# Performance work log

Measured on AMD Instinct MI355X. Metric: run time of the kernel, lower is better.

Reference implementation:

```python
import jax, jax.numpy as jnp
import numpy as np

DIM = 2048
HEADS = 32
WINDOW = 8   # local_attn
B = 4
N = 197


def _local_mask(w, n):
    # Faithful to local_attention(): for row i, columns j in [max(i-w,0), min(i+w, n))
    # get weight (w - |i-j|/2)/w; everything else is 0 (later masked to -inf).
    i = jnp.arange(n)[:, None]
    j = jnp.arange(n)[None, :]
    d = jnp.abs(i - j).astype(jnp.float32)
    in_win = (j >= i - w) & (j < i + w)  # range(start, end) excludes i+w
    return jnp.where(in_win, (w - d / 2.0) / w, 0.0)  # (N, N)


def setup_inputs() -> dict:
    key = jax.random.key(0)
    k1, k2, k3, k4 = jax.random.split(key, 4)
    x = jax.random.normal(k1, (B, N, DIM), dtype=jnp.float32)
    qkv_w = jax.random.normal(k2, (3 * DIM, DIM), dtype=jnp.float32) * 0.02  # no qkv bias
    proj_w = jax.random.normal(k3, (DIM, DIM), dtype=jnp.float32) * 0.02
    proj_b = jax.random.normal(k4, (DIM,), dtype=jnp.float32) * 0.02
    return {"x": x, "qkv_w": qkv_w, "proj_w": proj_w, "proj_b": proj_b}


def reference(x, qkv_w, proj_w, proj_b):
    Bb, Nn, C = x.shape
    H = HEADS
    hd = C // H
    scale = hd ** (-0.5)
    # qkv projection: (B, N, 3C) -> (3, B, H, N, hd)
    qkv = (x @ qkv_w.T).reshape(Bb, Nn, 3, H, hd).transpose(2, 0, 3, 1, 4)
    q, k, v = qkv[0], qkv[1], qkv[2]
    attn = jnp.einsum('bhnd,bhmd->bhnm', q, k) * scale  # (B, H, N, N)
    m = _local_mask(WINDOW, Nn)  # (N, N), broadcasts over B, H
    # attn * mask, then masked_fill(mask == 0, -inf), then softmax
    attn = jnp.where(m != 0.0, attn * m, -jnp.inf)
    attn = jax.nn.softmax(attn, axis=-1)
    out = jnp.einsum('bhnm,bhmd->bhnd', attn, v)  # (B, H, N, hd)
    out = out.transpose(0, 2, 1, 3).reshape(Bb, Nn, C)
    return out @ proj_w.T + proj_b
```

## Files before the change

kernel.cpp:

```cpp
#include <hip/hip_runtime.h>
#include <math.h>

#define B_SZ   4
#define N_SEQ  197
#define DIMC   2048
#define HEADS  32
#define HD     64
#define WIN    8
#define M_ROWS (B_SZ * N_SEQ)
#define M_PAD  896

using f32x4 = __attribute__((ext_vector_type(4))) float;
using s16x8 = __attribute__((ext_vector_type(8))) short;

__device__ inline ushort f2bf(float f) {
  uint x = __float_as_uint(f);
  uint r = (x + 0x7fffu + ((x >> 16) & 1u)) >> 16;
  return (ushort)r;
}
__device__ inline float bf2f(ushort u) {
  return __uint_as_float(((uint)u) << 16);
}

__device__ inline void gload16(const ushort* g, ushort* l) {
  __builtin_amdgcn_global_load_lds(
      (const __attribute__((address_space(1))) unsigned int*)g,
      (__attribute__((address_space(3))) unsigned int*)l, 16, 0, 0);
}

#define NX (M_ROWS * DIMC / 8)
#define NQ (3 * DIMC * DIMC / 8)
#define NP (DIMC * DIMC / 8)

__global__ __launch_bounds__(256)
void cvt_all(const float* __restrict__ x,  const float* __restrict__ qw,
             const float* __restrict__ pw, ushort* __restrict__ xb,
             ushort* __restrict__ qwb, ushort* __restrict__ pwb) {
  int i = blockIdx.x * 256 + threadIdx.x;
  const float* src; ushort* dst; int idx;
  if (i < NX)                { src = x;  dst = xb;  idx = i; }
  else if (i < NX + NQ)      { src = qw; dst = qwb; idx = i - NX; }
  else if (i < NX + NQ + NP) { src = pw; dst = pwb; idx = i - NX - NQ; }
  else return;
  f32x4 a = ((const f32x4*)src)[2 * idx];
  f32x4 b = ((const f32x4*)src)[2 * idx + 1];
  ushort4 u0, u1;
  u0.x = f2bf(a.x); u0.y = f2bf(a.y); u0.z = f2bf(a.z); u0.w = f2bf(a.w);
  u1.x = f2bf(b.x); u1.y = f2bf(b.y); u1.z = f2bf(b.z); u1.w = f2bf(b.w);
  ((ushort4*)dst)[2 * idx]     = u0;
  ((ushort4*)dst)[2 * idx + 1] = u1;
}

__global__ __launch_bounds__(256, 3)
void gemm_bt_bf16(const ushort* __restrict__ A, const ushort* __restrict__ Bw,
                  ushort* __restrict__ Cout,
                  int Mdim, int Ndim, int Kfull, int Ksplit) {
  __shared__ ushort As[3][128 * 32];
  __shared__ ushort Bs[3][128 * 32];
  const int tid  = threadIdx.x;
  const int lane = tid & 63;
  const int wave = tid >> 6;

  const int nwg  = gridDim.x * gridDim.y;
  const int phys = blockIdx.y * gridDim.x + blockIdx.x;
  const int cpx  = nwg >> 3;
  const int lg   = (phys & 7) * cpx + (phys >> 3);
  const int m0 = (lg % gridDim.x) * 128;
  const int n0 = (lg / gridDim.x) * 128;
  const int koff = blockIdx.z * Ksplit;
  ushort* C = Cout + (size_t)blockIdx.z * Mdim * Ndim;

  const int wr = (wave >> 1) * 64;
  const int wc = (wave & 1) * 64;
  const int fr = lane & 15;
  const int kg = lane >> 4;
  const int srow = lane >> 2;
  const int scol = ((lane & 3) ^ ((srow >> 1) & 3)) * 8;
  const int rdA  = (kg ^ ((fr >> 1) & 3)) * 8;

  f32x4 acc[4][4];
#pragma unroll
  for (int i = 0; i < 4; ++i)
#pragma unroll
    for (int j = 0; j < 4; ++j)
      acc[i][j] = (f32x4){0.f, 0.f, 0.f, 0.f};

  const ushort* Asrc0 = A  + (size_t)(m0 + wave * 32 + srow)      * Kfull + koff + scol;
  const ushort* Asrc1 = A  + (size_t)(m0 + wave * 32 + 16 + srow) * Kfull + koff + scol;
  const ushort* Bsrc0 = Bw + (size_t)(n0 + wave * 32 + srow)      * Kfull + koff + scol;
  const ushort* Bsrc1 = Bw + (size_t)(n0 + wave * 32 + 16 + srow) * Kfull + koff + scol;

  const int nt = Ksplit >> 5;

  auto STAGE = [&](int kk, int b) {
    const int k = kk << 5;
    gload16(Asrc0 + k, &As[b][wave * 1024]);
    gload16(Asrc1 + k, &As[b][wave * 1024 + 512]);
    gload16(Bsrc0 + k, &Bs[b][wave * 1024]);
    gload16(Bsrc1 + k, &Bs[b][wave * 1024 + 512]);
  };

  STAGE(0, 0);
  STAGE(1, 1);

  int cur = 0, s2 = 2;
  for (int t = 0; t < nt; ++t) {
    if (t < nt - 1) asm volatile("s_waitcnt vmcnt(4)" ::: "memory");
    else            asm volatile("s_waitcnt vmcnt(0)" ::: "memory");
    __builtin_amdgcn_s_barrier();
    __builtin_amdgcn_sched_barrier(0);

    if (t + 2 < nt) STAGE(t + 2, s2);

    s16x8 af[4], bfr[4];
#pragma unroll
    for (int i = 0; i < 4; ++i)
      af[i] = *(const s16x8*)(&As[cur][(wr + i * 16 + fr) * 32 + rdA]);
#pragma unroll
    for (int j = 0; j < 4; ++j)
      bfr[j] = *(const s16x8*)(&Bs[cur][(wc + j * 16 + fr) * 32 + rdA]);
    __builtin_amdgcn_s_setprio(1);
#pragma unroll
    for (int i = 0; i < 4; ++i)
#pragma unroll
      for (int j = 0; j < 4; ++j)
        acc[i][j] = __builtin_amdgcn_mfma_f32_16x16x32_bf16(af[i], bfr[j], acc[i][j], 0, 0, 0);
    __builtin_amdgcn_s_setprio(0);

    cur += 1; if (cur >= 3) cur -= 3;
    s2  += 1; if (s2  >= 3) s2  -= 3;
  }

  const int crow_base = m0 + wr + kg * 4;
  const int ccol_base = n0 + wc + fr;
#pragma unroll
  for (int j = 0; j < 4; ++j) {
    int col = ccol_base + j * 16;
#pragma unroll
    for (int i = 0; i < 4; ++i)
#pragma unroll
      for (int r = 0; r < 4; ++r) {
        int grow = crow_base + i * 16 + r;
        if (grow < Mdim) C[(size_t)grow * Ndim + col] = f2bf(acc[i][j][r]);
      }
  }
}

__global__ __launch_bounds__(256)
void local_attn(const ushort* __restrict__ p0, const ushort* __restrict__ p1,
                ushort* __restrict__ ao) {
  __shared__ float plds[4][16][68];
  const int wv = threadIdx.x >> 6;
  const int gw = blockIdx.x * 4 + wv;
  if (gw >= B_SZ * HEADS * N_SEQ) return;
  const int lane = threadIdx.x & 63;
  const int jj = lane >> 2;
  const int ds = lane & 3;
  const int h = gw % HEADS;
  const int t = gw / HEADS;
  const int i = t % N_SEQ;
  const int b = t / N_SEQ;
  const int row = b * N_SEQ + i;
  const size_t stride = 3 * DIMC;

  int j0 = i - WIN; if (j0 < 0) j0 = 0;
  int j1 = i + WIN; if (j1 > N_SEQ) j1 = N_SEQ;
  const int j = j0 + jj;
  const bool ok = (j < j1);
  const int jc = ok ? j : (j1 - 1);
  const size_t kvbase = (size_t)(b * N_SEQ + jc) * stride + h * HD + ds * 16;

  const ushort* vp0 = p0 + kvbase + 2 * DIMC;
  const ushort* vp1 = p1 + kvbase + 2 * DIMC;
  s16x8 va0 = *(const s16x8*)(vp0);
  s16x8 va1 = *(const s16x8*)(vp0 + 8);
  s16x8 vb0 = *(const s16x8*)(vp1);
  s16x8 vb1 = *(const s16x8*)(vp1 + 8);

  float qs[16];
  {
    const size_t qi = (size_t)row * stride + h * HD + ds * 16;
    s16x8 a0 = *(const s16x8*)(p0 + qi);
    s16x8 a1 = *(const s16x8*)(p0 + qi + 8);
    s16x8 b0 = *(const s16x8*)(p1 + qi);
    s16x8 b1 = *(const s16x8*)(p1 + qi + 8);
#pragma unroll
    for (int e = 0; e < 8; ++e) {
      qs[e]     = bf2f((ushort)a0[e]) + bf2f((ushort)b0[e]);
      qs[8 + e] = bf2f((ushort)a1[e]) + bf2f((ushort)b1[e]);
    }
  }

  float s;
  {
    const ushort* kp0 = p0 + kvbase + DIMC;
    const ushort* kp1 = p1 + kvbase + DIMC;
    s16x8 a0 = *(const s16x8*)(kp0);
    s16x8 a1 = *(const s16x8*)(kp0 + 8);
    s16x8 b0 = *(const s16x8*)(kp1);
    s16x8 b1 = *(const s16x8*)(kp1 + 8);
    float acc = 0.f;
#pragma unroll
    for (int e = 0; e < 8; ++e) {
      acc += qs[e]     * (bf2f((ushort)a0[e]) + bf2f((ushort)b0[e]));
      acc += qs[8 + e] * (bf2f((ushort)a1[e]) + bf2f((ushort)b1[e]));
    }
    s = acc;
  }
  s += __shfl_xor(s, 1);
  s += __shfl_xor(s, 2);

  {
    float d = fabsf((float)(i - j));
    float m = 1.0f - d * 0.0625f;
    s = ok ? s * (0.125f * m) : -INFINITY;
  }

  float mx = s;
  mx = fmaxf(mx, __shfl_xor(mx, 4));
  mx = fmaxf(mx, __shfl_xor(mx, 8));
  mx = fmaxf(mx, __shfl_xor(mx, 16));
  mx = fmaxf(mx, __shfl_xor(mx, 32));
  float e = __expf(s - mx);
  float sum = e;
  sum += __shfl_xor(sum, 4);
  sum += __shfl_xor(sum, 8);
  sum += __shfl_xor(sum, 16);
  sum += __shfl_xor(sum, 32);
  const float inv = 1.f / sum;

  {
    const float ee = ok ? e : 0.f;
    f32x4 w0, w1, w2, w3;
#pragma unroll
    for (int g = 0; g < 4; ++g) {
      w0[g] = ee * (bf2f((ushort)va0[g])     + bf2f((ushort)vb0[g]));
      w1[g] = ee * (bf2f((ushort)va0[4 + g]) + bf2f((ushort)vb0[4 + g]));
      w2[g] = ee * (bf2f((ushort)va1[g])     + bf2f((ushort)vb1[g]));
      w3[g] = ee * (bf2f((ushort)va1[4 + g]) + bf2f((ushort)vb1[4 + g]));
    }
    *(f32x4*)&plds[wv][jj][ds * 16]      = w0;
    *(f32x4*)&plds[wv][jj][ds * 16 + 4]  = w1;
    *(f32x4*)&plds[wv][jj][ds * 16 + 8]  = w2;
    *(f32x4*)&plds[wv][jj][ds * 16 + 12] = w3;
  }
  asm volatile("s_waitcnt lgkmcnt(0)" ::: "memory");
  __builtin_amdgcn_sched_barrier(0);

  float o = 0.f;
#pragma unroll
  for (int q = 0; q < 16; ++q) o += plds[wv][q][lane];
  ao[(size_t)row * DIMC + h * HD + lane] = f2bf(o * inv);
}

#define NR8 (M_ROWS * DIMC / 8)
__global__ __launch_bounds__(256)
void reduce4_bias(const ushort* __restrict__ parts, const float* __restrict__ bias,
                  float* __restrict__ out) {
  int i = blockIdx.x * 256 + threadIdx.x;
  if (i >= NR8) return;
  const size_t slice = (size_t)M_ROWS * DIMC;
  float a[8];
#pragma unroll
  for (int e = 0; e < 8; ++e) a[e] = 0.f;
#pragma unroll
  for (int z = 0; z < 4; ++z) {
    s16x8 v = *(const s16x8*)(parts + z * slice + (size_t)i * 8);
#pragma unroll
    for (int e = 0; e < 8; ++e) a[e] += bf2f((ushort)v[e]);
  }
  const int col = (i * 8) & (DIMC - 1);
  f32x4 b0 = *(const f32x4*)(bias + col);
  f32x4 b1 = *(const f32x4*)(bias + col + 4);
  f32x4 o0 = {a[0] + b0.x, a[1] + b0.y, a[2] + b0.z, a[3] + b0.w};
  f32x4 o1 = {a[4] + b1.x, a[5] + b1.y, a[6] + b1.z, a[7] + b1.w};
  ((f32x4*)out)[2 * i]     = o0;
  ((f32x4*)out)[2 * i + 1] = o1;
}

extern "C" void kernel_launch(void* const* d_in, const int* in_sizes, int n_in,
                              void* d_out, int out_size, void* d_ws, size_t ws_size,
                              hipStream_t stream) {
  const float* x      = (const float*)d_in[0];
  const float* qkv_w  = (const float*)d_in[1];
  const float* proj_w = (const float*)d_in[2];
  const float* proj_b = (const float*)d_in[3];
  float* out = (float*)d_out;

  char* p = (char*)d_ws;
  ushort* x_bf    = (ushort*)p;  p += (size_t)M_PAD * DIMC * 2;
  ushort* qkvw_bf = (ushort*)p;  p += (size_t)3 * DIMC * DIMC * 2;
  ushort* projw_bf= (ushort*)p;  p += (size_t)DIMC * DIMC * 2;
  ushort* qkv_p   = (ushort*)p;  p += (size_t)2 * M_ROWS * 3 * DIMC * 2;
  ushort* ao_bf   = (ushort*)p;  p += (size_t)M_PAD * DIMC * 2;
  ushort* proj_p  = (ushort*)p;

  dim3 blk(256);

  {
    int total = NX + NQ + NP;
    cvt_all<<<dim3((total + 255) / 256), blk, 0, stream>>>(
        x, qkv_w, proj_w, x_bf, qkvw_bf, projw_bf);
  }

  gemm_bt_bf16<<<dim3(M_PAD / 128, (3 * DIMC) / 128, 2), blk, 0, stream>>>(
      x_bf, qkvw_bf, qkv_p, M_ROWS, 3 * DIMC, DIMC, DIMC / 2);

  int total_waves = B_SZ * HEADS * N_SEQ;
  local_attn<<<dim3((total_waves + 3) / 4), blk, 0, stream>>>(
      qkv_p, qkv_p + (size_t)M_ROWS * 3 * DIMC, ao_bf);

  gemm_bt_bf16<<<dim3(M_PAD / 128, DIMC / 128, 4), blk, 0, stream>>>(
      ao_bf, projw_bf, proj_p, M_ROWS, DIMC, DIMC, DIMC / 4);

  reduce4_bias<<<dim3((NR8 + 255) / 256), blk, 0, stream>>>(proj_p, proj_b, out);
}
```

Before: 87.97 us.

## Fuse split-K reduction and bias into projection GEMM via last-block atomic counter

Removes the separate reduce4_bias kernel. Each output tile of the split-K projection GEMM bumps an atomic counter once its partial is written, and the last z-slice block to arrive sums the bf16 partials, adds the bias and writes the fp32 output. The counters are zeroed inside the existing conversion kernel. This saves one kernel launch and lets the reduction read partials that are likely still in cache, at the cost of thread fences, an atomic per block, and reduction work concentrated in the last-arriving blocks.

```diff
diff --git a/kernel.cpp b/kernel.cpp
--- a/kernel.cpp
+++ b/kernel.cpp
@@ -31,16 +31,19 @@
 #define NX (M_ROWS * DIMC / 8)
 #define NQ (3 * DIMC * DIMC / 8)
 #define NP (DIMC * DIMC / 8)
+#define NCNT 112
 
 __global__ __launch_bounds__(256)
 void cvt_all(const float* __restrict__ x,  const float* __restrict__ qw,
              const float* __restrict__ pw, ushort* __restrict__ xb,
-             ushort* __restrict__ qwb, ushort* __restrict__ pwb) {
+             ushort* __restrict__ qwb, ushort* __restrict__ pwb,
+             int* __restrict__ cnt) {
   int i = blockIdx.x * 256 + threadIdx.x;
   const float* src; ushort* dst; int idx;
   if (i < NX)                { src = x;  dst = xb;  idx = i; }
   else if (i < NX + NQ)      { src = qw; dst = qwb; idx = i - NX; }
   else if (i < NX + NQ + NP) { src = pw; dst = pwb; idx = i - NX - NQ; }
+  else if (i < NX + NQ + NP + NCNT) { cnt[i - NX - NQ - NP] = 0; return; }
   else return;
   f32x4 a = ((const f32x4*)src)[2 * idx];
   f32x4 b = ((const f32x4*)src)[2 * idx + 1];
@@ -51,12 +54,16 @@
   ((ushort4*)dst)[2 * idx + 1] = u1;
 }
 
+template<int FUSERED>
 __global__ __launch_bounds__(256, 3)
 void gemm_bt_bf16(const ushort* __restrict__ A, const ushort* __restrict__ Bw,
                   ushort* __restrict__ Cout,
-                  int Mdim, int Ndim, int Kfull, int Ksplit) {
+                  int Mdim, int Ndim, int Kfull, int Ksplit,
+                  float* __restrict__ Cfinal, const float* __restrict__ bias,
+                  int* __restrict__ cnt, int zcount) {
   __shared__ ushort As[3][128 * 32];
   __shared__ ushort Bs[3][128 * 32];
+  __shared__ int lastFlag;
   const int tid  = threadIdx.x;
   const int lane = tid & 63;
   const int wave = tid >> 6;
@@ -143,6 +150,41 @@
         int grow = crow_base + i * 16 + r;
         if (grow < Mdim) C[(size_t)grow * Ndim + col] = f2bf(acc[i][j][r]);
       }
+  }
+
+  if constexpr (FUSERED) {
+    __threadfence();
+    __syncthreads();
+    if (tid == 0) {
+      int old = atomicAdd(&cnt[phys], 1);
+      lastFlag = (old == zcount - 1);
+    }
+    __syncthreads();
+    if (!lastFlag) return;
+    __threadfence();
+
+    const size_t slice = (size_t)Mdim * Ndim;
+    for (int g = tid; g < 2048; g += 256) {
+      const int r = g >> 4;
+      const int grow = m0 + r;
+      if (grow >= Mdim) continue;
+      const int gcol = n0 + (g & 15) * 8;
+      const size_t off = (size_t)grow * Ndim + gcol;
+      float a[8];
+#pragma unroll
+      for (int e = 0; e < 8; ++e) a[e] = 0.f;
+      for (int z = 0; z < zcount; ++z) {
+        s16x8 v = *(const s16x8*)(Cout + z * slice + off);
+#pragma unroll
+        for (int e = 0; e < 8; ++e) a[e] += bf2f((ushort)v[e]);
+      }
+      f32x4 b0 = *(const f32x4*)(bias + gcol);
+      f32x4 b1 = *(const f32x4*)(bias + gcol + 4);
+      f32x4 o0 = {a[0] + b0.x, a[1] + b0.y, a[2] + b0.z, a[3] + b0.w};
+      f32x4 o1 = {a[4] + b1.x, a[5] + b1.y, a[6] + b1.z, a[7] + b1.w};
+      *(f32x4*)(Cfinal + off)     = o0;
+      *(f32x4*)(Cfinal + off + 4) = o1;
+    }
   }
 }
 
@@ -253,31 +295,6 @@
   ao[(size_t)row * DIMC + h * HD + lane] = f2bf(o * inv);
 }
 
-#define NR8 (M_ROWS * DIMC / 8)
-__global__ __launch_bounds__(256)
-void reduce4_bias(const ushort* __restrict__ parts, const float* __restrict__ bias,
-                  float* __restrict__ out) {
-  int i = blockIdx.x * 256 + threadIdx.x;
-  if (i >= NR8) return;
-  const size_t slice = (size_t)M_ROWS * DIMC;
-  float a[8];
-#pragma unroll
-  for (int e = 0; e < 8; ++e) a[e] = 0.f;
-#pragma unroll
-  for (int z = 0; z < 4; ++z) {
-    s16x8 v = *(const s16x8*)(parts + z * slice + (size_t)i * 8);
-#pragma unroll
-    for (int e = 0; e < 8; ++e) a[e] += bf2f((ushort)v[e]);
-  }
-  const int col = (i * 8) & (DIMC - 1);
-  f32x4 b0 = *(const f32x4*)(bias + col);
-  f32x4 b1 = *(const f32x4*)(bias + col + 4);
-  f32x4 o0 = {a[0] + b0.x, a[1] + b0.y, a[2] + b0.z, a[3] + b0.w};
-  f32x4 o1 = {a[4] + b1.x, a[5] + b1.y, a[6] + b1.z, a[7] + b1.w};
-  ((f32x4*)out)[2 * i]     = o0;
-  ((f32x4*)out)[2 * i + 1] = o1;
-}
-
 extern "C" void kernel_launch(void* const* d_in, const int* in_sizes, int n_in,
                               void* d_out, int out_size, void* d_ws, size_t ws_size,
                               hipStream_t stream) {
@@ -293,25 +310,26 @@
   ushort* projw_bf= (ushort*)p;  p += (size_t)DIMC * DIMC * 2;
   ushort* qkv_p   = (ushort*)p;  p += (size_t)2 * M_ROWS * 3 * DIMC * 2;
   ushort* ao_bf   = (ushort*)p;  p += (size_t)M_PAD * DIMC * 2;
-  ushort* proj_p  = (ushort*)p;
+  ushort* proj_p  = (ushort*)p;  p += (size_t)4 * M_ROWS * DIMC * 2;
+  int*    cnt     = (int*)p;
 
   dim3 blk(256);
 
   {
-    int total = NX + NQ + NP;
+    int total = NX + NQ + NP + NCNT;
     cvt_all<<<dim3((total + 255) / 256), blk, 0, stream>>>(
-        x, qkv_w, proj_w, x_bf, qkvw_bf, projw_bf);
-  }
-
-  gemm_bt_bf16<<<dim3(M_PAD / 128, (3 * DIMC) / 128, 2), blk, 0, stream>>>(
-      x_bf, qkvw_bf, qkv_p, M_ROWS, 3 * DIMC, DIMC, DIMC / 2);
+        x, qkv_w, proj_w, x_bf, qkvw_bf, projw_bf, cnt);
+  }
+
+  gemm_bt_bf16<0><<<dim3(M_PAD / 128, (3 * DIMC) / 128, 2), blk, 0, stream>>>(
+      x_bf, qkvw_bf, qkv_p, M_ROWS, 3 * DIMC, DIMC, DIMC / 2,
+      nullptr, nullptr, nullptr, 2);
 
   int total_waves = B_SZ * HEADS * N_SEQ;
   local_attn<<<dim3((total_waves + 3) / 4), blk, 0, stream>>>(
       qkv_p, qkv_p + (size_t)M_ROWS * 3 * DIMC, ao_bf);
 
-  gemm_bt_bf16<<<dim3(M_PAD / 128, DIMC / 128, 4), blk, 0, stream>>>(
-      ao_bf, projw_bf, proj_p, M_ROWS, DIMC, DIMC, DIMC / 4);
-
-  reduce4_bias<<<dim3((NR8 + 255) / 256), blk, 0, stream>>>(proj_p, proj_b, out);
-}
+  gemm_bt_bf16<1><<<dim3(M_PAD / 128, DIMC / 128, 4), blk, 0, stream>>>(
+      ao_bf, projw_bf, proj_p, M_ROWS, DIMC, DIMC, DIMC / 4,
+      out, proj_b, cnt, 4);
+}
```

New measurement: 163.8 us. 86.2% more time.
